# Performance work log

Hardware: AMD Instinct MI355X
Metric: run time of the kernel (lower is better)

The kernel has to match this reference:

```python
import jax, jax.numpy as jnp
import numpy as np


def _ln(x, g, b, eps=1e-5):
    m = x.mean(-1, keepdims=True)
    v = x.var(-1, keepdims=True)
    return (x - m) / jnp.sqrt(v + eps) * g + b


def setup_inputs() -> dict:
    key = jax.random.key(0)
    ks = jax.random.split(key, 12)
    B, N, F, D, DI = 1024, 100000, 128, 256, 512

    def w(k, shape, fan_in):
        return jax.random.normal(k, shape, jnp.float32) / np.sqrt(fan_in).astype(np.float32)

    return {
        "x_num": jax.random.normal(ks[0], (B, F), jnp.float32),
        "cand_num": jax.random.normal(ks[1], (N, F), jnp.float32),
        "cand_y": jax.random.normal(ks[2], (N, 1), jnp.float32),
        "W_lin": w(ks[3], (F, D), F), "b_lin": jnp.zeros(D, jnp.float32),
        "W_K": w(ks[4], (D, D), D), "b_K": jnp.zeros(D, jnp.float32),
        "W_Y": w(ks[5], (1, D), 2), "b_Y": jnp.zeros(D, jnp.float32),
        "W_T1": w(ks[6], (D, DI), D), "b_T1": jnp.zeros(DI, jnp.float32),
        "W_T2": w(ks[7], (DI, D), DI),
        "ln_p_g": jnp.ones(D, jnp.float32), "ln_p_b": jnp.zeros(D, jnp.float32),
        "W_P1": w(ks[8], (D, DI), D), "b_P1": jnp.zeros(DI, jnp.float32),
        "W_P2": w(ks[9], (DI, D), DI), "b_P2": jnp.zeros(D, jnp.float32),
        "ln_o_g": jnp.ones(D, jnp.float32), "ln_o_b": jnp.zeros(D, jnp.float32),
        "W_out": w(ks[10], (D, 1), D), "b_out": jnp.zeros(1, jnp.float32),
        "context_size": 96,
    }


def reference(x_num, cand_num, cand_y,
              W_lin, b_lin, W_K, b_K, W_Y, b_Y,
              W_T1, b_T1, W_T2,
              ln_p_g, ln_p_b, W_P1, b_P1, W_P2, b_P2,
              ln_o_g, ln_o_b, W_out, b_out,
              context_size):
    # Encoder (encoder_n_blocks=0, normlization=None -> identity f)
    x_enc = x_num @ W_lin + b_lin                       # [B, D]
    k = x_enc @ W_K + b_K                               # [B, D]
    # Candidate keys (computed under torch.no_grad in the original)
    ki_all = jax.lax.stop_gradient((cand_num @ W_lin + b_lin) @ W_K + b_K)  # [N, D]

    # Exact brute-force L2 kNN == faiss.IndexFlatL2
    d2 = (k * k).sum(-1, keepdims=True) - 2.0 * (k @ ki_all.T) + (ki_all * ki_all).sum(-1)  # [B, N]
    _, I = jax.lax.top_k(-d2, context_size)             # [B, C] ascending distance
    ki = ki_all[I]                                      # [B, C, D]

    # S = ||k - ki||^2 per the source formula; softmax over context
    S = (k * k).sum(-1, keepdims=True) \
        - 2.0 * jnp.einsum('bd,bcd->bc', k, ki) \
        + (ki * ki).sum(-1)                             # [B, C]
    weights = jax.nn.softmax(S, axis=-1)                # context_dropout=0 (eval)

    encode_y = cand_y[I] @ W_Y + b_Y                    # [B, C, D]
    diff = k[:, None, :] - ki                           # [B, C, D]
    V = encode_y + jax.nn.relu(diff @ W_T1 + b_T1) @ W_T2  # T MLP, no bias on 2nd linear
    V = jnp.einsum('bc,bcd->bd', weights, V)            # weighted context reduction

    x = x_enc + V
    # predictor residual block: LN -> Linear -> ReLU -> Linear
    h = _ln(x, ln_p_g, ln_p_b)
    x = x + (jax.nn.relu(h @ W_P1 + b_P1) @ W_P2 + b_P2)
    # head P: LN -> ReLU -> Linear(d, 1)
    return jax.nn.relu(_ln(x, ln_o_g, ln_o_b)) @ W_out + b_out  # [B, 1]
```

## Files before the change

### kernel.cpp

```cpp
#include <hip/hip_runtime.h>
#include <math.h>

#define BQ 1024
#define FDIM 128
#define DDIM 256
#define DIDIM 512
#define NTOT 100000
#define NP 100096
#define NCVT 12512
#define CTX 96
#define CAP 8192
#define MSUB 12288
#define RSUB 48
#define LBUF 1280
#define CSTR 16

typedef _Float16 f16x8 __attribute__((ext_vector_type(8)));
typedef _Float16 f16x4 __attribute__((ext_vector_type(4)));
typedef float f32x4 __attribute__((ext_vector_type(4)));

__global__ __launch_bounds__(256) void k_prep(
    const float* __restrict__ cand, _Float16* __restrict__ c2,
    const float* __restrict__ Wlin, const float* __restrict__ blin,
    const float* __restrict__ WK, const float* __restrict__ bK,
    const float* __restrict__ WT1,
    float* __restrict__ Wf, float* __restrict__ bf, float* __restrict__ WfT1)
{
    int blk = blockIdx.x, tid = threadIdx.x;
    if (blk < NCVT) {
        int t = blk*256 + tid;
        int row = t >> 5;
        int c4 = (t & 31) * 4;
        float4 v = {0.f, 0.f, 0.f, 0.f};
        if (row < NTOT) v = *(const float4*)(cand + (size_t)row*FDIM + c4);
        float vv[4] = {v.x, v.y, v.z, v.w};
        f16x4 h, hs, l;
        #pragma unroll
        for (int q = 0; q < 4; ++q) {
            _Float16 hq = (_Float16)vv[q];
            float hf = (float)hq;
            h[q]  = hq;
            hs[q] = (_Float16)(hf * 0.015625f);
            l[q]  = (_Float16)((vv[q] - hf) * 64.f);
        }
        size_t b = (size_t)row*384 + c4;
        *(f16x4*)(c2 + b)       = h;
        *(f16x4*)(c2 + b + 128) = hs;
        *(f16x4*)(c2 + b + 256) = l;
        return;
    }
    int i = blk - NCVT;
    __shared__ float red[256];
    int j = tid;
    if (i < FDIM) {
        float acc = 0.f;
        for (int l = 0; l < DDIM; ++l) acc += Wlin[i*DDIM + l] * WK[l*DDIM + j];
        Wf[i*DDIM + j] = acc;
        red[j] = acc;
        __syncthreads();
        float a0 = 0.f, a1 = 0.f;
        for (int l = 0; l < DDIM; ++l) {
            float w = red[l];
            a0 += w * WT1[(size_t)l*DIDIM + j];
            a1 += w * WT1[(size_t)l*DIDIM + j + 256];
        }
        WfT1[(size_t)i*DIDIM + j] = a0;
        WfT1[(size_t)i*DIDIM + j + 256] = a1;
    } else {
        float acc = bK[j];
        for (int l = 0; l < DDIM; ++l) acc += blin[l] * WK[l*DDIM + j];
        bf[j] = acc;
        red[j] = acc*acc; __syncthreads();
        for (int s2 = 128; s2 > 0; s2 >>= 1) { if (j < s2) red[j] += red[j+s2]; __syncthreads(); }
        if (j == 0) bf[256] = red[0];
    }
}

__global__ __launch_bounds__(256) void k_prep2(
    const float* __restrict__ x, const float* __restrict__ Wlin,
    const float* __restrict__ blin, const float* __restrict__ Wf,
    const float* __restrict__ bf, const float* __restrict__ WfT1,
    const float* __restrict__ bT1,
    float* __restrict__ xenc, float* __restrict__ kp,
    _Float16* __restrict__ kp2, float* __restrict__ xP,
    _Float16* __restrict__ Wsp)
{
    __shared__ float xs[FDIM];
    __shared__ float ks[DDIM];
    int blk = blockIdx.x, tid = threadIdx.x;
    if (blk >= BQ) {
        int jj = (blk - BQ)*2 + (tid >> 7);
        int l = tid & 127;
        float w = (jj < DDIM) ? Wf[l*DDIM + jj] : WfT1[(size_t)l*DIDIM + (jj - DDIM)];
        _Float16 h = (_Float16)w;
        float hf = (float)h;
        Wsp[(size_t)jj*384 + l]       = h;
        Wsp[(size_t)jj*384 + 128 + l] = (_Float16)((w - hf) * 64.f);
        Wsp[(size_t)jj*384 + 256 + l] = (_Float16)(hf * 0.015625f);
        return;
    }
    int b = blk, j = tid;
    if (j < FDIM) xs[j] = x[(size_t)b*FDIM + j];
    __syncthreads();
    float a0 = blin[j], a1 = bf[j];
    for (int l = 0; l < FDIM; ++l) {
        float xv = xs[l];
        a0 += xv * Wlin[l*DDIM + j];
        a1 += xv * Wf[l*DDIM + j];
    }
    xenc[(size_t)b*DDIM + j] = a0;
    ks[j] = a1;
    float p0 = bT1[j], p1 = bT1[j + 256];
    for (int l = 0; l < FDIM; ++l) {
        float xv = xs[l];
        p0 += xv * WfT1[(size_t)l*DIDIM + j];
        p1 += xv * WfT1[(size_t)l*DIDIM + j + 256];
    }
    xP[(size_t)b*DIDIM + j] = p0;
    xP[(size_t)b*DIDIM + j + 256] = p1;
    __syncthreads();
    if (j < FDIM) {
        float a = 0.f;
        for (int d = 0; d < DDIM; ++d) a += Wf[j*DDIM + d] * ks[d];
        kp[(size_t)b*FDIM + j] = a;
        _Float16 h = (_Float16)a;
        float hf = (float)h;
        kp2[(size_t)b*384 + j]       = h;
        kp2[(size_t)b*384 + 128 + j] = (_Float16)((a - hf) * 64.f);
        kp2[(size_t)b*384 + 256 + j] = (_Float16)(hf * 0.015625f);
    }
}

__global__ __launch_bounds__(256) void k_cnorm(
    const _Float16* __restrict__ A, const _Float16* __restrict__ B,
    float* __restrict__ knp, const float* __restrict__ bf)
{
    __shared__ __align__(16) _Float16 As[128*64];
    __shared__ __align__(16) _Float16 Bs[128*64];
    int tid = threadIdx.x;
    int lane = tid & 63, wv = tid >> 6;
    int wm = wv >> 1, wn = wv & 1;
    int bn = blockIdx.x * 128;
    int bm = blockIdx.y * 128;
    f32x4 acc[4][4] = {};
    const size_t baseA = (size_t)bm * 384;
    const size_t baseB = (size_t)bn * 384;
    for (int kt = 0; kt < 6; ++kt) {
        #pragma unroll
        for (int r = 0; r < 4; ++r) {
            int w = wv*4 + r;
            int s = w*64 + lane;
            int rl = s & 15;
            int q  = (s >> 4) & 3;
            int kk2= (s >> 6) & 1;
            int ii = (s >> 7) & 3;
            int wq = (s >> 9) & 1;
            size_t goff = (size_t)(wq*64 + ii*16 + rl)*384 + kt*64 + (kk2*4 + q)*8;
            __builtin_amdgcn_global_load_lds(
                (const __attribute__((address_space(1))) void*)(A + baseA + goff),
                (__attribute__((address_space(3))) void*)(As + w*512), 16, 0, 0);
            __builtin_amdgcn_global_load_lds(
                (const __attribute__((address_space(1))) void*)(B + baseB + goff),
                (__attribute__((address_space(3))) void*)(Bs + w*512), 16, 0, 0);
        }
        __syncthreads();
        #pragma unroll
        for (int kk = 0; kk < 2; ++kk) {
            f16x8 af[4], bfr[4];
            #pragma unroll
            for (int i = 0; i < 4; ++i)
                af[i] = *(const f16x8*)&As[((wm*8 + i*2 + kk)*64 + (lane>>4)*16 + (lane&15))*8];
            #pragma unroll
            for (int j = 0; j < 4; ++j)
                bfr[j] = *(const f16x8*)&Bs[((wn*8 + j*2 + kk)*64 + (lane>>4)*16 + (lane&15))*8];
            #pragma unroll
            for (int i = 0; i < 4; ++i)
                #pragma unroll
                for (int j = 0; j < 4; ++j)
                    acc[i][j] = __builtin_amdgcn_mfma_f32_16x16x32_f16(af[i], bfr[j], acc[i][j], 0, 0, 0);
        }
        __syncthreads();
    }
    float bfv[4];
    #pragma unroll
    for (int j = 0; j < 4; ++j) bfv[j] = bf[bn + wn*64 + j*16 + (lane&15)];
    int bnt = bn >> 7;
    #pragma unroll
    for (int i = 0; i < 4; ++i) {
        #pragma unroll
        for (int rg = 0; rg < 4; ++rg) {
            float s = 0.f;
            #pragma unroll
            for (int j = 0; j < 4; ++j) {
                float q = acc[i][j][rg];
                s += q * (q + 2.f*bfv[j]);
            }
            s += __shfl_xor(s, 1, 64);
            s += __shfl_xor(s, 2, 64);
            s += __shfl_xor(s, 4, 64);
            s += __shfl_xor(s, 8, 64);
            if ((lane & 15) == 0) {
                int row = bm + wm*64 + i*16 + (lane>>4)*4 + rg;
                knp[(size_t)(bnt*2 + wn)*NP + row] = s;
            }
        }
    }
}

__global__ __launch_bounds__(256) void k_norm_fin(
    const float* __restrict__ knp, const float* __restrict__ bf, float* __restrict__ kinorm)
{
    int n = blockIdx.x*256 + threadIdx.x;
    kinorm[n] = (n < NTOT)
        ? bf[256] + knp[n] + knp[(size_t)NP + n] + knp[(size_t)2*NP + n] + knp[(size_t)3*NP + n]
        : INFINITY;
}

__global__ __launch_bounds__(256) void k_mini(
    const _Float16* __restrict__ kp2, const _Float16* __restrict__ cand2,
    const float* __restrict__ kinorm, _Float16* __restrict__ msb)
{
    __shared__ __align__(16) _Float16 As[128*64];
    __shared__ __align__(16) _Float16 Bs[128*64];
    int tid = threadIdx.x;
    int lane = tid & 63, wv = tid >> 6;
    int wm = wv >> 1, wn = wv & 1;
    int bm = blockIdx.x * 128;
    int bn = blockIdx.y * 128;
    f32x4 acc[4][4] = {};
    const size_t baseA = (size_t)bm * 384;
    const size_t baseB = (size_t)bn * 384;
    for (int kt = 0; kt < 2; ++kt) {
        #pragma unroll
        for (int r = 0; r < 4; ++r) {
            int w = wv*4 + r;
            int s = w*64 + lane;
            int rl = s & 15;
            int q  = (s >> 4) & 3;
            int kk2= (s >> 6) & 1;
            int ii = (s >> 7) & 3;
            int wq = (s >> 9) & 1;
            size_t goff = (size_t)(wq*64 + ii*16 + rl)*384 + kt*64 + (kk2*4 + q)*8;
            __builtin_amdgcn_global_load_lds(
                (const __attribute__((address_space(1))) void*)(kp2 + baseA + goff),
                (__attribute__((address_space(3))) void*)(As + w*512), 16, 0, 0);
            __builtin_amdgcn_global_load_lds(
                (const __attribute__((address_space(1))) void*)(cand2 + baseB + goff),
                (__attribute__((address_space(3))) void*)(Bs + w*512), 16, 0, 0);
        }
        __syncthreads();
        #pragma unroll
        for (int kk = 0; kk < 2; ++kk) {
            f16x8 af[4], bfr[4];
            #pragma unroll
            for (int i = 0; i < 4; ++i)
                af[i] = *(const f16x8*)&As[((wm*8 + i*2 + kk)*64 + (lane>>4)*16 + (lane&15))*8];
            #pragma unroll
            for (int j = 0; j < 4; ++j)
                bfr[j] = *(const f16x8*)&Bs[((wn*8 + j*2 + kk)*64 + (lane>>4)*16 + (lane&15))*8];
            #pragma unroll
            for (int i = 0; i < 4; ++i)
                #pragma unroll
                for (int j = 0; j < 4; ++j)
                    acc[i][j] = __builtin_amdgcn_mfma_f32_16x16x32_f16(af[i], bfr[j], acc[i][j], 0, 0, 0);
        }
        __syncthreads();
    }
    #pragma unroll
    for (int i = 0; i < 4; ++i) {
        int m = bm + wm*64 + i*16 + (lane>>4)*4;
        #pragma unroll
        for (int j = 0; j < 4; ++j) {
            int nl = bn + wn*64 + j*16 + (lane&15);
            float kn = kinorm[nl];
            #pragma unroll
            for (int rg = 0; rg < 4; ++rg)
                msb[(size_t)(m + rg)*MSUB + nl] = (_Float16)fmaxf(kn - 2.f*acc[i][j][rg], 0.f);
        }
    }
}

__global__ __launch_bounds__(256) void k_subT(
    const unsigned short* __restrict__ msb, int* __restrict__ Tq, int* __restrict__ cnt)
{
    __shared__ unsigned h[1024];
    __shared__ unsigned pr[256];
    __shared__ unsigned h2[64];
    __shared__ int tstar;
    __shared__ unsigned cbel;
    int b = blockIdx.x, tid = threadIdx.x;
    if (tid == 0) cnt[b*CSTR] = 0;
    #pragma unroll
    for (int i = 0; i < 4; ++i) h[tid + i*256] = 0;
    if (tid == 0) tstar = 1023;
    if (tid < 64) h2[tid] = 0;
    __syncthreads();
    const unsigned short* row = msb + (size_t)b*MSUB;
    for (int base = 0; base < MSUB; base += 2048) {
        uint4 u = *(const uint4*)(row + base + tid*8);
        atomicAdd(&h[(u.x & 0xffffu) >> 6], 1u);
        atomicAdd(&h[(u.x >> 16) >> 6], 1u);
        atomicAdd(&h[(u.y & 0xffffu) >> 6], 1u);
        atomicAdd(&h[(u.y >> 16) >> 6], 1u);
        atomicAdd(&h[(u.z & 0xffffu) >> 6], 1u);
        atomicAdd(&h[(u.z >> 16) >> 6], 1u);
        atomicAdd(&h[(u.w & 0xffffu) >> 6], 1u);
        atomicAdd(&h[(u.w >> 16) >> 6], 1u);
    }
    __syncthreads();
    unsigned s0 = h[tid*4], s1 = h[tid*4+1], s2 = h[tid*4+2], s3 = h[tid*4+3];
    unsigned tot = s0 + s1 + s2 + s3;
    pr[tid] = tot;
    __syncthreads();
    for (int off = 1; off < 256; off <<= 1) {
        unsigned t2 = (tid >= off) ? pr[tid - off] : 0;
        __syncthreads();
        pr[tid] += t2;
        __syncthreads();
    }
    unsigned c = pr[tid] - tot;
    int found = -1;
    c += s0; if (c >= RSUB) found = tid*4;
    if (found < 0) { c += s1; if (c >= RSUB) found = tid*4+1; }
    if (found < 0) { c += s2; if (c >= RSUB) found = tid*4+2; }
    if (found < 0) { c += s3; if (c >= RSUB) found = tid*4+3; }
    if (found >= 0) atomicMin(&tstar, found);
    __syncthreads();
    if (tid == (tstar >> 2)) {
        unsigned below = pr[tid] - tot;
        int pos = tstar & 3;
        if (pos > 0) below += s0;
        if (pos > 1) below += s1;
        if (pos > 2) below += s2;
        cbel = below;
    }
    __syncthreads();
    int ts = tstar;
    for (int base = 0; base < MSUB; base += 2048) {
        uint4 u = *(const uint4*)(row + base + tid*8);
        unsigned e[8] = { u.x & 0xffffu, u.x >> 16, u.y & 0xffffu, u.y >> 16,
                          u.z & 0xffffu, u.z >> 16, u.w & 0xffffu, u.w >> 16 };
        #pragma unroll
        for (int q = 0; q < 8; ++q)
            if ((int)(e[q] >> 6) == ts) atomicAdd(&h2[e[q] & 63], 1u);
    }
    __syncthreads();
    if (tid == 0) {
        unsigned cum = cbel; int code = 63;
        for (int i = 0; i < 64; ++i) { cum += h2[i]; if (cum >= RSUB) { code = i; break; } }
        Tq[b] = (ts << 6) + code;
    }
}

__global__ __launch_bounds__(256) void k_dist_mfma(
    const _Float16* __restrict__ kp2, const _Float16* __restrict__ cand2,
    const float* __restrict__ kinorm, const int* __restrict__ Tq,
    int* __restrict__ cnt, int* __restrict__ candI)
{
    __shared__ __align__(16) _Float16 As[128*64];
    __shared__ __align__(16) _Float16 Bs[128*64];
    __shared__ int lcnt;
    __shared__ unsigned lbuf[LBUF];
    __shared__ float kns[128];
    __shared__ int tqss[128];
    int tid = threadIdx.x;
    int lane = tid & 63, wv = tid >> 6;
    int wm = wv >> 1, wn = wv & 1;
    int r0 = blockIdx.x & 7, u0 = blockIdx.x >> 3;
    int pq = r0*782 + u0;
    int bm = (pq & 7) * 128;
    int bn = (pq >> 3) * 128;
    if (tid == 0) lcnt = 0;
    if (tid < 128) { kns[tid] = kinorm[bn + tid]; tqss[tid] = Tq[bm + tid]; }
    f32x4 acc[4][4] = {};
    const size_t baseA = (size_t)bm * 384;
    const size_t baseB = (size_t)bn * 384;
    for (int kt = 0; kt < 2; ++kt) {
        #pragma unroll
        for (int r = 0; r < 4; ++r) {
            int w = wv*4 + r;
            int s = w*64 + lane;
            int rl = s & 15;
            int q  = (s >> 4) & 3;
            int kk2= (s >> 6) & 1;
            int ii = (s >> 7) & 3;
            int wq = (s >> 9) & 1;
            size_t goff = (size_t)(wq*64 + ii*16 + rl)*384 + kt*64 + (kk2*4 + q)*8;
            __builtin_amdgcn_global_load_lds(
                (const __attribute__((address_space(1))) void*)(kp2 + baseA + goff),
                (__attribute__((address_space(3))) void*)(As + w*512), 16, 0, 0);
            __builtin_amdgcn_global_load_lds(
                (const __attribute__((address_space(1))) void*)(cand2 + baseB + goff),
                (__attribute__((address_space(3))) void*)(Bs + w*512), 16, 0, 0);
        }
        __syncthreads();
        #pragma unroll
        for (int kk = 0; kk < 2; ++kk) {
            f16x8 af[4], bfr[4];
            #pragma unroll
            for (int i = 0; i < 4; ++i)
                af[i] = *(const f16x8*)&As[((wm*8 + i*2 + kk)*64 + (lane>>4)*16 + (lane&15))*8];
            #pragma unroll
            for (int j = 0; j < 4; ++j)
                bfr[j] = *(const f16x8*)&Bs[((wn*8 + j*2 + kk)*64 + (lane>>4)*16 + (lane&15))*8];
            #pragma unroll
            for (int i = 0; i < 4; ++i)
                #pragma unroll
                for (int j = 0; j < 4; ++j)
                    acc[i][j] = __builtin_amdgcn_mfma_f32_16x16x32_f16(af[i], bfr[j], acc[i][j], 0, 0, 0);
        }
        __syncthreads();
    }
    #pragma unroll
    for (int i = 0; i < 4; ++i) {
        int m0 = bm + wm*64 + i*16 + (lane>>4)*4;
        int lrow = wm*64 + i*16 + (lane>>4)*4;
        int tqs[4];
        #pragma unroll
        for (int rg = 0; rg < 4; ++rg) tqs[rg] = tqss[lrow + rg];
        #pragma unroll
        for (int j = 0; j < 4; ++j) {
            int lcol = wn*64 + j*16 + (lane&15);
            int nl = bn + lcol;
            float kn = kns[lcol];
            #pragma unroll
            for (int rg = 0; rg < 4; ++rg) {
                float sc = fmaxf(kn - 2.f*acc[i][j][rg], 0.f);
                _Float16 k16 = (_Float16)sc;
                unsigned short kb;
                __builtin_memcpy(&kb, &k16, 2);
                if (kb <= (unsigned short)tqs[rg]) {
                    int p = atomicAdd(&lcnt, 1);
                    if (p < LBUF) lbuf[p] = ((unsigned)(m0 + rg) << 17) | (unsigned)nl;
                    else {
                        int pp = atomicAdd(&cnt[(m0 + rg)*CSTR], 1);
                        if (pp < CAP) candI[(size_t)(m0 + rg)*CAP + pp] = nl;
                    }
                }
            }
        }
    }
    __syncthreads();
    int c = lcnt < LBUF ? lcnt : LBUF;
    for (int i2 = tid; i2 < c; i2 += 256) {
        unsigned pk = lbuf[i2];
        int row = pk >> 17, col = (int)(pk & 0x1ffffu);
        int pp = atomicAdd(&cnt[row*CSTR], 1);
        if (pp < CAP) candI[(size_t)row*CAP + pp] = col;
    }
}

__device__ __forceinline__ float row_score(
    const float* __restrict__ cand, const float* kps, const float* __restrict__ kinorm, int n)
{
    float acc0 = 0.f, acc1 = 0.f;
    #pragma unroll 4
    for (int d = 0; d < FDIM; d += 8) {
        float4 v0 = *(const float4*)(cand + (size_t)n*FDIM + d);
        float4 v1 = *(const float4*)(cand + (size_t)n*FDIM + d + 4);
        acc0 += v0.x*kps[d]   + v0.y*kps[d+1] + v0.z*kps[d+2] + v0.w*kps[d+3];
        acc1 += v1.x*kps[d+4] + v1.y*kps[d+5] + v1.z*kps[d+6] + v1.w*kps[d+7];
    }
    return kinorm[n] - 2.f*(acc0 + acc1);
}

__global__ __launch_bounds__(256) void k_fix(
    const float* __restrict__ kp, const float* __restrict__ cand,
    const float* __restrict__ kinorm, int* __restrict__ cnt, int* __restrict__ candI)
{
    __shared__ float kps[FDIM];
    __shared__ unsigned h[1024];
    __shared__ unsigned pr[256];
    __shared__ unsigned h2[64];
    __shared__ int tstar;
    __shared__ unsigned cbel;
    __shared__ unsigned Tsh;
    int b = blockIdx.x, tid = threadIdx.x;
    int c0 = cnt[b*CSTR];
    if (c0 >= CTX && c0 <= CAP) return;
    if (tid < FDIM) kps[tid] = kp[(size_t)b*FDIM + tid];
    #pragma unroll
    for (int i = 0; i < 4; ++i) h[tid + i*256] = 0;
    if (tid == 0) tstar = 1023;
    if (tid < 64) h2[tid] = 0;
    __syncthreads();
    for (int n = tid; n < NTOT; n += 256) {
        float sc = fmaxf(row_score(cand, kps, kinorm, n), 0.f);
        _Float16 k16 = (_Float16)sc;
        unsigned short kb; __builtin_memcpy(&kb, &k16, 2);
        atomicAdd(&h[kb >> 6], 1u);
    }
    __syncthreads();
    unsigned s0 = h[tid*4], s1 = h[tid*4+1], s2 = h[tid*4+2], s3 = h[tid*4+3];
    unsigned tot = s0 + s1 + s2 + s3;
    pr[tid] = tot;
    __syncthreads();
    for (int off = 1; off < 256; off <<= 1) {
        unsigned t2 = (tid >= off) ? pr[tid - off] : 0;
        __syncthreads();
        pr[tid] += t2;
        __syncthreads();
    }
    unsigned c = pr[tid] - tot;
    int found = -1;
    c += s0; if (c >= CTX) found = tid*4;
    if (found < 0) { c += s1; if (c >= CTX) found = tid*4+1; }
    if (found < 0) { c += s2; if (c >= CTX) found = tid*4+2; }
    if (found < 0) { c += s3; if (c >= CTX) found = tid*4+3; }
    if (found >= 0) atomicMin(&tstar, found);
    __syncthreads();
    if (tid == (tstar >> 2)) {
        unsigned below = pr[tid] - tot;
        int pos = tstar & 3;
        if (pos > 0) below += s0;
        if (pos > 1) below += s1;
        if (pos > 2) below += s2;
        cbel = below;
    }
    __syncthreads();
    int ts = tstar;
    for (int n = tid; n < NTOT; n += 256) {
        float sc = fmaxf(row_score(cand, kps, kinorm, n), 0.f);
        _Float16 k16 = (_Float16)sc;
        unsigned short kb; __builtin_memcpy(&kb, &k16, 2);
        if ((int)((unsigned)kb >> 6) == ts) atomicAdd(&h2[kb & 63], 1u);
    }
    __syncthreads();
    if (tid == 0) {
        unsigned cum = cbel; int code = 63;
        for (int i = 0; i < 64; ++i) { cum += h2[i]; if (cum >= CTX) { code = i; break; } }
        Tsh = (unsigned)((ts << 6) + code);
        cnt[b*CSTR] = 0;
    }
    __syncthreads();
    unsigned T2 = Tsh;
    for (int n = tid; n < NTOT; n += 256) {
        float sc = fmaxf(row_score(cand, kps, kinorm, n), 0.f);
        _Float16 k16 = (_Float16)sc;
        unsigned short kb; __builtin_memcpy(&kb, &k16, 2);
        if ((unsigned)kb <= T2) {
            int pp = atomicAdd(&cnt[b*CSTR], 1);
            if (pp < CAP) candI[(size_t)b*CAP + pp] = n;
        }
    }
}

__global__ __launch_bounds__(256) void k_resc(
    const float* __restrict__ kp, const float* __restrict__ cand,
    const float* __restrict__ kinorm, const int* __restrict__ cnt,
    const int* __restrict__ candI, const float* __restrict__ candy,
    int* __restrict__ finI, float* __restrict__ wts, float* __restrict__ wy)
{
    __shared__ float kps[FDIM];
    __shared__ float sval[2048];
    __shared__ int   sidx[2048];
    __shared__ float sh[256];
    int b = blockIdx.x, tid = threadIdx.x;
    if (tid < FDIM) kps[tid] = kp[(size_t)b*FDIM + tid];
    if (tid < 128) { sval[tid] = INFINITY; sidx[tid] = 0x7fffffff; }
    int nc = cnt[b*CSTR]; if (nc > CAP) nc = CAP;
    __syncthreads();
    for (int c0 = 0; c0 < nc; c0 += 1920) {
        int m = nc - c0; if (m > 1920) m = 1920;
        for (int c = tid; c < m; c += 256) {
            int n = candI[(size_t)b*CAP + c0 + c];
            sval[128 + c] = row_score(cand, kps, kinorm, n);
            sidx[128 + c] = n;
        }
        __syncthreads();
        int nv = 128 + m;
        int size = 256; while (size < nv) size <<= 1;
        for (int i2 = nv + tid; i2 < size; i2 += 256) { sval[i2] = INFINITY; sidx[i2] = 0x7fffffff; }
        __syncthreads();
        for (int k2 = 2; k2 <= size; k2 <<= 1) {
            for (int jj = k2 >> 1; jj > 0; jj >>= 1) {
                for (int i = tid; i < size; i += 256) {
                    int ix = i ^ jj;
                    if (ix > i) {
                        bool up = ((i & k2) == 0);
                        float a = sval[i], b2 = sval[ix];
                        int ia = sidx[i], ib = sidx[ix];
                        bool gt = (a > b2) || (a == b2 && ia > ib);
                        if (gt == up) {
                            sval[i] = b2; sval[ix] = a;
                            sidx[i] = ib; sidx[ix] = ia;
                        }
                    }
                }
                __syncthreads();
            }
        }
    }
    if (tid < CTX) finI[(size_t)b*CTX + tid] = sidx[tid];
    float m = sval[CTX-1];
    float e = (tid < CTX) ? expf(sval[tid] - m) : 0.f;
    sh[tid] = e;
    __syncthreads();
    for (int s2 = 128; s2 > 0; s2 >>= 1) { if (tid < s2) sh[tid] += sh[tid+s2]; __syncthreads(); }
    float sum = sh[0];
    __syncthreads();
    float w = e / sum;
    if (tid < CTX) wts[(size_t)b*CTX + tid] = w;
    sh[tid] = (tid < CTX) ? w * candy[sidx[tid]] : 0.f;
    __syncthreads();
    for (int s2 = 128; s2 > 0; s2 >>= 1) { if (tid < s2) sh[tid] += sh[tid+s2]; __syncthreads(); }
    if (tid == 0) wy[b] = sh[0];
}

__global__ __launch_bounds__(256) void k_tmlp2(
    const _Float16* __restrict__ c2, const _Float16* __restrict__ Wsp,
    const float* __restrict__ xP,
    const int* __restrict__ finI, const float* __restrict__ wts,
    float* __restrict__ Hw)
{
    __shared__ __align__(16) _Float16 As[768*8];
    __shared__ __align__(16) _Float16 Bs[1024*8];
    __shared__ int   idx[CTX];
    __shared__ float wsh[CTX];
    int b = blockIdx.x, ct = blockIdx.y;
    int tid = threadIdx.x;
    int lane = tid & 63, wv = tid >> 6;
    if (tid < CTX) { idx[tid] = finI[b*CTX + tid]; wsh[tid] = wts[b*CTX + tid]; }
    __syncthreads();
    f32x4 acc[6][2] = {};
    const _Float16* Wbase = Wsp + (size_t)(DDIM + ct*128) * 384;
    for (int kt = 0; kt < 2; ++kt) {
        #pragma unroll
        for (int w = 0; w < 3; ++w) {
            int s = (wv*3 + w)*64 + lane;
            int rl = s & 15, q = (s >> 4) & 3, kk2 = (s >> 6) & 1, ii = s >> 7;
            int grow = idx[ii*16 + rl];
            __builtin_amdgcn_global_load_lds(
                (const __attribute__((address_space(1))) void*)(c2 + (size_t)grow*384 + kt*64 + (kk2*4 + q)*8),
                (__attribute__((address_space(3))) void*)(As + (size_t)s*8), 16, 0, 0);
        }
        #pragma unroll
        for (int w = 0; w < 4; ++w) {
            int s = (wv*4 + w)*64 + lane;
            int rl = s & 15, q = (s >> 4) & 3, kk2 = (s >> 6) & 1, jj = s >> 7;
            __builtin_amdgcn_global_load_lds(
                (const __attribute__((address_space(1))) void*)(Wbase + (size_t)(jj*16 + rl)*384 + kt*64 + (kk2*4 + q)*8),
                (__attribute__((address_space(3))) void*)(Bs + (size_t)s*8), 16, 0, 0);
        }
        __syncthreads();
        #pragma unroll
        for (int kk = 0; kk < 2; ++kk) {
            f16x8 bfr[2];
            #pragma unroll
            for (int j = 0; j < 2; ++j)
                bfr[j] = *(const f16x8*)&Bs[(((wv*2 + j)*2 + kk)*64 + (lane>>4)*16 + (lane&15))*8];
            #pragma unroll
            for (int i = 0; i < 6; ++i) {
                f16x8 af = *(const f16x8*)&As[((i*2 + kk)*64 + (lane>>4)*16 + (lane&15))*8];
                #pragma unroll
                for (int j = 0; j < 2; ++j)
                    acc[i][j] = __builtin_amdgcn_mfma_f32_16x16x32_f16(af, bfr[j], acc[i][j], 0, 0, 0);
            }
        }
        __syncthreads();
    }
    #pragma unroll
    for (int j = 0; j < 2; ++j) {
        int col = ct*128 + wv*32 + j*16 + (lane & 15);
        float xv = xP[(size_t)b*DIDIM + col];
        float p = 0.f;
        #pragma unroll
        for (int i = 0; i < 6; ++i) {
            #pragma unroll
            for (int rg = 0; rg < 4; ++rg) {
                int row = i*16 + (lane>>4)*4 + rg;
                p += wsh[row] * fmaxf(xv - acc[i][j][rg], 0.f);
            }
        }
        p += __shfl_xor(p, 16, 64);
        p += __shfl_xor(p, 32, 64);
        if ((lane >> 4) == 0) Hw[(size_t)b*DIDIM + col] = p;
    }
}

__device__ __forceinline__ float bsum(float v, float* red, int j)
{
    red[j] = v; __syncthreads();
    if (j < 64) {
        float t = red[j] + red[j+64] + red[j+128] + red[j+192];
        #pragma unroll
        for (int o2 = 32; o2; o2 >>= 1) t += __shfl_xor(t, o2, 64);
        if (j == 0) red[0] = t;
    }
    __syncthreads();
    float t = red[0];
    __syncthreads();
    return t;
}

__global__ __launch_bounds__(256) void k_final4(
    const float* __restrict__ xenc, const float* __restrict__ Hw,
    const float* __restrict__ wy,
    const float* __restrict__ WY, const float* __restrict__ bY,
    const float* __restrict__ WT2,
    const float* __restrict__ lpg, const float* __restrict__ lpb,
    const float* __restrict__ WP1, const float* __restrict__ bP1,
    const float* __restrict__ WP2, const float* __restrict__ bP2,
    const float* __restrict__ logg, const float* __restrict__ lob,
    const float* __restrict__ Wout, const float* __restrict__ bout,
    float* __restrict__ out)
{
    __shared__ float hs[4][DIDIM];
    __shared__ float xs[4][DDIM];
    __shared__ float red[256];
    int b0 = blockIdx.x*4, j = threadIdx.x;
    #pragma unroll
    for (int r = 0; r < 4; ++r) {
        hs[r][j] = Hw[(size_t)(b0+r)*DIDIM + j];
        hs[r][j+256] = Hw[(size_t)(b0+r)*DIDIM + j + 256];
    }
    __syncthreads();
    float v[4];
    #pragma unroll
    for (int r = 0; r < 4; ++r) v[r] = wy[b0+r]*WY[j] + bY[j];
    for (int dd = 0; dd < DIDIM; ++dd) {
        float w = WT2[dd*DDIM + j];
        #pragma unroll
        for (int r = 0; r < 4; ++r) v[r] += hs[r][dd]*w;
    }
    float x[4];
    #pragma unroll
    for (int r = 0; r < 4; ++r) x[r] = xenc[(size_t)(b0+r)*DDIM + j] + v[r];
    #pragma unroll
    for (int r = 0; r < 4; ++r) {
        float mean = bsum(x[r], red, j) * (1.f/DDIM);
        float xc = x[r] - mean;
        float var = bsum(xc*xc, red, j) * (1.f/DDIM);
        float rstd = 1.f / sqrtf(var + 1e-5f);
        xs[r][j] = xc * rstd * lpg[j] + lpb[j];
    }
    __syncthreads();
    float u0[4], u1[4];
    #pragma unroll
    for (int r = 0; r < 4; ++r) { u0[r] = bP1[j]; u1[r] = bP1[j+256]; }
    for (int dd = 0; dd < DDIM; ++dd) {
        float w0 = WP1[(size_t)dd*DIDIM + j], w1 = WP1[(size_t)dd*DIDIM + j + 256];
        #pragma unroll
        for (int r = 0; r < 4; ++r) { float hd = xs[r][dd]; u0[r] += hd*w0; u1[r] += hd*w1; }
    }
    __syncthreads();
    #pragma unroll
    for (int r = 0; r < 4; ++r) { hs[r][j] = fmaxf(u0[r], 0.f); hs[r][j+256] = fmaxf(u1[r], 0.f); }
    __syncthreads();
    float x2[4];
    #pragma unroll
    for (int r = 0; r < 4; ++r) x2[r] = x[r] + bP2[j];
    for (int dd = 0; dd < DIDIM; ++dd) {
        float w = WP2[dd*DDIM + j];
        #pragma unroll
        for (int r = 0; r < 4; ++r) x2[r] += hs[r][dd]*w;
    }
    #pragma unroll
    for (int r = 0; r < 4; ++r) {
        float mean = bsum(x2[r], red, j) * (1.f/DDIM);
        float xc = x2[r] - mean;
        float var = bsum(xc*xc, red, j) * (1.f/DDIM);
        float rstd = 1.f / sqrtf(var + 1e-5f);
        float rr = fmaxf(xc * rstd * logg[j] + lob[j], 0.f);
        float s = bsum(rr * Wout[j], red, j);
        if (j == 0) out[b0+r] = s + bout[0];
    }
}

extern "C" void kernel_launch(void* const* d_in, const int* in_sizes, int n_in,
                              void* d_out, int out_size, void* d_ws, size_t ws_size,
                              hipStream_t stream)
{
    (void)in_sizes; (void)n_in; (void)out_size; (void)ws_size;
    const float* x_num = (const float*)d_in[0];
    const float* cand  = (const float*)d_in[1];
    const float* candy = (const float*)d_in[2];
    const float* Wlin  = (const float*)d_in[3];
    const float* blin  = (const float*)d_in[4];
    const float* WK    = (const float*)d_in[5];
    const float* bK    = (const float*)d_in[6];
    const float* WY    = (const float*)d_in[7];
    const float* bY    = (const float*)d_in[8];
    const float* WT1   = (const float*)d_in[9];
    const float* bT1   = (const float*)d_in[10];
    const float* WT2   = (const float*)d_in[11];
    const float* lpg   = (const float*)d_in[12];
    const float* lpb   = (const float*)d_in[13];
    const float* WP1   = (const float*)d_in[14];
    const float* bP1   = (const float*)d_in[15];
    const float* WP2   = (const float*)d_in[16];
    const float* bP2   = (const float*)d_in[17];
    const float* logg  = (const float*)d_in[18];
    const float* lob   = (const float*)d_in[19];
    const float* Wout  = (const float*)d_in[20];
    const float* bout  = (const float*)d_in[21];
    float* out = (float*)d_out;

    float* ws = (float*)d_ws;
    size_t o = 0;
    float* Wf     = ws + o; o += (size_t)FDIM*DDIM;
    float* bf     = ws + o; o += 320;
    float* WfT1   = ws + o; o += (size_t)FDIM*DIDIM;
    float* xenc   = ws + o; o += (size_t)BQ*DDIM;
    float* kp     = ws + o; o += (size_t)BQ*FDIM;
    float* kinorm = ws + o; o += NP;
    float* knp    = ws + o; o += (size_t)4*NP;
    int*   finI   = (int*)(ws + o); o += (size_t)BQ*CTX;
    float* wts    = ws + o; o += (size_t)BQ*CTX;
    float* wy     = ws + o; o += BQ;
    int*   Tq     = (int*)(ws + o); o += BQ;
    float* Hw     = ws + o; o += (size_t)BQ*DIDIM;
    float* xP     = ws + o; o += (size_t)BQ*DIDIM;
    _Float16* kp2 = (_Float16*)(ws + o); o += (size_t)BQ*384/2;
    _Float16* c2  = (_Float16*)(ws + o); o += (size_t)NP*384/2;
    _Float16* Wsp = (_Float16*)(ws + o); o += (size_t)768*384/2;
    int*   cnt    = (int*)(ws + o); o += (size_t)BQ*CSTR;
    int*   candI  = (int*)(ws + o); o += (size_t)BQ*CAP;
    _Float16* msb = (_Float16*)(ws + o); o += (size_t)BQ*MSUB;

    k_prep<<<dim3(NCVT + FDIM + 1), dim3(256), 0, stream>>>(
        cand, c2, Wlin, blin, WK, bK, WT1, Wf, bf, WfT1);
    k_prep2<<<dim3(BQ + 384), dim3(256), 0, stream>>>(
        x_num, Wlin, blin, Wf, bf, WfT1, bT1, xenc, kp, kp2, xP, Wsp);

    k_cnorm<<<dim3(DDIM/128, NP/128), dim3(256), 0, stream>>>(c2, Wsp, knp, bf);
    k_norm_fin<<<dim3(NP/256), dim3(256), 0, stream>>>(knp, bf, kinorm);

    k_mini<<<dim3(BQ/128, MSUB/128), dim3(256), 0, stream>>>(kp2, c2, kinorm, msb);
    k_subT<<<dim3(BQ), dim3(256), 0, stream>>>((const unsigned short*)msb, Tq, cnt);

    k_dist_mfma<<<dim3((BQ/128)*(NP/128)), dim3(256), 0, stream>>>(kp2, c2, kinorm, Tq, cnt, candI);
    k_fix<<<dim3(BQ), dim3(256), 0, stream>>>(kp, cand, kinorm, cnt, candI);
    k_resc<<<dim3(BQ), dim3(256), 0, stream>>>(kp, cand, kinorm, cnt, candI, candy,
                                               finI, wts, wy);

    k_tmlp2<<<dim3(BQ, 4), dim3(256), 0, stream>>>(c2, Wsp, xP, finI, wts, Hw);
    k_final4<<<dim3(BQ/4), dim3(256), 0, stream>>>(xenc, Hw, wy, WY, bY, WT2,
                                                   lpg, lpb, WP1, bP1, WP2, bP2,
                                                   logg, lob, Wout, bout, out);
}
```

Measured before the change: 404.0 us.

## Replace scalar final MLP kernel with split-fp16 MFMA GEMMs and LN kernels

The fused scalar FP32 kernel that ran the T2 projection, predictor MLP and output head is split into three MFMA GEMM kernels plus two per-row LayerNorm kernels. Activations and the weights WT2, WP1 and WP2 are packed into a three-part fp16 split (high, scaled high, scaled residual) so that fp16 MFMA can approximate fp32 accuracy, with weight packing added to the prep kernel. The aim is to remove the scalar FMA bottleneck in the tail. In exchange it adds extra launches, intermediate global buffers, and tiny grids (16 to 32 blocks) that may underfill the GPU.

```diff
diff --git a/kernel.cpp b/kernel.cpp
--- a/kernel.cpp
+++ b/kernel.cpp
@@ -8,6 +8,7 @@
 #define NTOT 100000
 #define NP 100096
 #define NCVT 12512
+#define NPACK 1024
 #define CTX 96
 #define CAP 8192
 #define MSUB 12288
@@ -15,6 +16,10 @@
 #define LBUF 1280
 #define CSTR 16
 
+#define WT2OFF 0
+#define WP1OFF (256*1536)
+#define WP2OFF (WP1OFF + 512*768)
+
 typedef _Float16 f16x8 __attribute__((ext_vector_type(8)));
 typedef _Float16 f16x4 __attribute__((ext_vector_type(4)));
 typedef float f32x4 __attribute__((ext_vector_type(4)));
@@ -24,7 +29,10 @@
     const float* __restrict__ Wlin, const float* __restrict__ blin,
     const float* __restrict__ WK, const float* __restrict__ bK,
     const float* __restrict__ WT1,
-    float* __restrict__ Wf, float* __restrict__ bf, float* __restrict__ WfT1)
+    const float* __restrict__ WT2, const float* __restrict__ WP1,
+    const float* __restrict__ WP2,
+    float* __restrict__ Wf, float* __restrict__ bf, float* __restrict__ WfT1,
+    _Float16* __restrict__ Wfin)
 {
     int blk = blockIdx.x, tid = threadIdx.x;
     if (blk < NCVT) {
@@ -50,6 +58,22 @@
         return;
     }
     int i = blk - NCVT;
+    if (i > FDIM) {
+        int c = i - FDIM - 1;
+        const float* W; int K, N, cl; size_t base;
+        if (c < 256)      { W = WT2; K = 512; N = 256; cl = c;     base = (size_t)WT2OFF + (size_t)c*1536; }
+        else if (c < 768) { W = WP1; K = 256; N = 512; cl = c-256; base = (size_t)WP1OFF + (size_t)(c-256)*768; }
+        else              { W = WP2; K = 512; N = 256; cl = c-768; base = (size_t)WP2OFF + (size_t)(c-768)*1536; }
+        for (int k = tid; k < K; k += 256) {
+            float w = W[(size_t)k*N + cl];
+            _Float16 h = (_Float16)w;
+            float hf = (float)h;
+            Wfin[base + k]       = h;
+            Wfin[base + K + k]   = (_Float16)((w - hf) * 64.f);
+            Wfin[base + 2*K + k] = (_Float16)(hf * 0.015625f);
+        }
+        return;
+    }
     __shared__ float red[256];
     int j = tid;
     if (i < FDIM) {
@@ -611,7 +635,7 @@
     const _Float16* __restrict__ c2, const _Float16* __restrict__ Wsp,
     const float* __restrict__ xP,
     const int* __restrict__ finI, const float* __restrict__ wts,
-    float* __restrict__ Hw)
+    _Float16* __restrict__ Hw2)
 {
     __shared__ __align__(16) _Float16 As[768*8];
     __shared__ __align__(16) _Float16 Bs[1024*8];
@@ -674,7 +698,13 @@
         }
         p += __shfl_xor(p, 16, 64);
         p += __shfl_xor(p, 32, 64);
-        if ((lane >> 4) == 0) Hw[(size_t)b*DIDIM + col] = p;
+        if ((lane >> 4) == 0) {
+            _Float16 h = (_Float16)p;
+            float hf = (float)h;
+            Hw2[(size_t)b*1536 + col]        = h;
+            Hw2[(size_t)b*1536 + 512 + col]  = (_Float16)(hf * 0.015625f);
+            Hw2[(size_t)b*1536 + 1024 + col] = (_Float16)((p - hf) * 64.f);
+        }
     }
 }
 
@@ -693,78 +723,234 @@
     return t;
 }
 
-__global__ __launch_bounds__(256) void k_final4(
-    const float* __restrict__ xenc, const float* __restrict__ Hw,
-    const float* __restrict__ wy,
+__global__ __launch_bounds__(256) void k_g1(
+    const _Float16* __restrict__ Hw2, const _Float16* __restrict__ Wfin,
+    const float* __restrict__ xenc, const float* __restrict__ wy,
     const float* __restrict__ WY, const float* __restrict__ bY,
-    const float* __restrict__ WT2,
-    const float* __restrict__ lpg, const float* __restrict__ lpb,
-    const float* __restrict__ WP1, const float* __restrict__ bP1,
-    const float* __restrict__ WP2, const float* __restrict__ bP2,
-    const float* __restrict__ logg, const float* __restrict__ lob,
-    const float* __restrict__ Wout, const float* __restrict__ bout,
-    float* __restrict__ out)
-{
-    __shared__ float hs[4][DIDIM];
-    __shared__ float xs[4][DDIM];
+    float* __restrict__ xbuf)
+{
+    __shared__ __align__(16) _Float16 As[128*64];
+    __shared__ __align__(16) _Float16 Bs[128*64];
+    int tid = threadIdx.x;
+    int lane = tid & 63, wv = tid >> 6;
+    int wm = wv >> 1, wn = wv & 1;
+    int bn = blockIdx.x * 128;
+    int bm = blockIdx.y * 128;
+    f32x4 acc[4][4] = {};
+    const size_t baseA = (size_t)bm * 1536;
+    const size_t baseB = (size_t)WT2OFF + (size_t)bn * 1536;
+    for (int kt = 0; kt < 24; ++kt) {
+        #pragma unroll
+        for (int r = 0; r < 4; ++r) {
+            int w = wv*4 + r;
+            int s = w*64 + lane;
+            int rl = s & 15, q = (s>>4)&3, kk2 = (s>>6)&1, ii = (s>>7)&3, wq = (s>>9)&1;
+            size_t goff = (size_t)(wq*64 + ii*16 + rl)*1536 + kt*64 + (kk2*4 + q)*8;
+            __builtin_amdgcn_global_load_lds(
+                (const __attribute__((address_space(1))) void*)(Hw2 + baseA + goff),
+                (__attribute__((address_space(3))) void*)(As + w*512), 16, 0, 0);
+            __builtin_amdgcn_global_load_lds(
+                (const __attribute__((address_space(1))) void*)(Wfin + baseB + goff),
+                (__attribute__((address_space(3))) void*)(Bs + w*512), 16, 0, 0);
+        }
+        __syncthreads();
+        #pragma unroll
+        for (int kk = 0; kk < 2; ++kk) {
+            f16x8 af[4], bfr[4];
+            #pragma unroll
+            for (int i = 0; i < 4; ++i)
+                af[i] = *(const f16x8*)&As[((wm*8 + i*2 + kk)*64 + (lane>>4)*16 + (lane&15))*8];
+            #pragma unroll
+            for (int j = 0; j < 4; ++j)
+                bfr[j] = *(const f16x8*)&Bs[((wn*8 + j*2 + kk)*64 + (lane>>4)*16 + (lane&15))*8];
+            #pragma unroll
+            for (int i = 0; i < 4; ++i)
+                #pragma unroll
+                for (int j = 0; j < 4; ++j)
+                    acc[i][j] = __builtin_amdgcn_mfma_f32_16x16x32_f16(af[i], bfr[j], acc[i][j], 0, 0, 0);
+        }
+        __syncthreads();
+    }
+    #pragma unroll
+    for (int i = 0; i < 4; ++i) {
+        int m = bm + wm*64 + i*16 + (lane>>4)*4;
+        #pragma unroll
+        for (int j = 0; j < 4; ++j) {
+            int n = bn + wn*64 + j*16 + (lane&15);
+            #pragma unroll
+            for (int rg = 0; rg < 4; ++rg) {
+                int row = m + rg;
+                float val = acc[i][j][rg] + xenc[(size_t)row*DDIM + n] + wy[row]*WY[n] + bY[n];
+                xbuf[(size_t)row*DDIM + n] = val;
+            }
+        }
+    }
+}
+
+__global__ __launch_bounds__(256) void k_ln1(
+    const float* __restrict__ xbuf, const float* __restrict__ lpg,
+    const float* __restrict__ lpb, _Float16* __restrict__ xs2)
+{
     __shared__ float red[256];
-    int b0 = blockIdx.x*4, j = threadIdx.x;
+    int b = blockIdx.x, j = threadIdx.x;
+    float x = xbuf[(size_t)b*DDIM + j];
+    float mean = bsum(x, red, j) * (1.f/DDIM);
+    float xc = x - mean;
+    float var = bsum(xc*xc, red, j) * (1.f/DDIM);
+    float rstd = 1.f / sqrtf(var + 1e-5f);
+    float v = xc * rstd * lpg[j] + lpb[j];
+    _Float16 h = (_Float16)v;
+    float hf = (float)h;
+    xs2[(size_t)b*768 + j]       = h;
+    xs2[(size_t)b*768 + 256 + j] = (_Float16)(hf * 0.015625f);
+    xs2[(size_t)b*768 + 512 + j] = (_Float16)((v - hf) * 64.f);
+}
+
+__global__ __launch_bounds__(256) void k_g2(
+    const _Float16* __restrict__ xs2, const _Float16* __restrict__ Wfin,
+    const float* __restrict__ bP1, _Float16* __restrict__ U2)
+{
+    __shared__ __align__(16) _Float16 As[128*64];
+    __shared__ __align__(16) _Float16 Bs[128*64];
+    int tid = threadIdx.x;
+    int lane = tid & 63, wv = tid >> 6;
+    int wm = wv >> 1, wn = wv & 1;
+    int bn = blockIdx.x * 128;
+    int bm = blockIdx.y * 128;
+    f32x4 acc[4][4] = {};
+    const size_t baseA = (size_t)bm * 768;
+    const size_t baseB = (size_t)WP1OFF + (size_t)bn * 768;
+    for (int kt = 0; kt < 12; ++kt) {
+        #pragma unroll
+        for (int r = 0; r < 4; ++r) {
+            int w = wv*4 + r;
+            int s = w*64 + lane;
+            int rl = s & 15, q = (s>>4)&3, kk2 = (s>>6)&1, ii = (s>>7)&3, wq = (s>>9)&1;
+            size_t goff = (size_t)(wq*64 + ii*16 + rl)*768 + kt*64 + (kk2*4 + q)*8;
+            __builtin_amdgcn_global_load_lds(
+                (const __attribute__((address_space(1))) void*)(xs2 + baseA + goff),
+                (__attribute__((address_space(3))) void*)(As + w*512), 16, 0, 0);
+            __builtin_amdgcn_global_load_lds(
+                (const __attribute__((address_space(1))) void*)(Wfin + baseB + goff),
+                (__attribute__((address_space(3))) void*)(Bs + w*512), 16, 0, 0);
+        }
+        __syncthreads();
+        #pragma unroll
+        for (int kk = 0; kk < 2; ++kk) {
+            f16x8 af[4], bfr[4];
+            #pragma unroll
+            for (int i = 0; i < 4; ++i)
+                af[i] = *(const f16x8*)&As[((wm*8 + i*2 + kk)*64 + (lane>>4)*16 + (lane&15))*8];
+            #pragma unroll
+            for (int j = 0; j < 4; ++j)
+                bfr[j] = *(const f16x8*)&Bs[((wn*8 + j*2 + kk)*64 + (lane>>4)*16 + (lane&15))*8];
+            #pragma unroll
+            for (int i = 0; i < 4; ++i)
+                #pragma unroll
+                for (int j = 0; j < 4; ++j)
+                    acc[i][j] = __builtin_amdgcn_mfma_f32_16x16x32_f16(af[i], bfr[j], acc[i][j], 0, 0, 0);
+        }
+        __syncthreads();
+    }
     #pragma unroll
-    for (int r = 0; r < 4; ++r) {
-        hs[r][j] = Hw[(size_t)(b0+r)*DIDIM + j];
-        hs[r][j+256] = Hw[(size_t)(b0+r)*DIDIM + j + 256];
-    }
-    __syncthreads();
-    float v[4];
+    for (int i = 0; i < 4; ++i) {
+        int m = bm + wm*64 + i*16 + (lane>>4)*4;
+        #pragma unroll
+        for (int j = 0; j < 4; ++j) {
+            int n = bn + wn*64 + j*16 + (lane&15);
+            float bv = bP1[n];
+            #pragma unroll
+            for (int rg = 0; rg < 4; ++rg) {
+                int row = m + rg;
+                float r = fmaxf(acc[i][j][rg] + bv, 0.f);
+                _Float16 h = (_Float16)r;
+                float hf = (float)h;
+                U2[(size_t)row*1536 + n]        = h;
+                U2[(size_t)row*1536 + 512 + n]  = (_Float16)(hf * 0.015625f);
+                U2[(size_t)row*1536 + 1024 + n] = (_Float16)((r - hf) * 64.f);
+            }
+        }
+    }
+}
+
+__global__ __launch_bounds__(256) void k_g3(
+    const _Float16* __restrict__ U2, const _Float16* __restrict__ Wfin,
+    const float* __restrict__ xbuf, const float* __restrict__ bP2,
+    float* __restrict__ x2buf)
+{
+    __shared__ __align__(16) _Float16 As[128*64];
+    __shared__ __align__(16) _Float16 Bs[128*64];
+    int tid = threadIdx.x;
+    int lane = tid & 63, wv = tid >> 6;
+    int wm = wv >> 1, wn = wv & 1;
+    int bn = blockIdx.x * 128;
+    int bm = blockIdx.y * 128;
+    f32x4 acc[4][4] = {};
+    const size_t baseA = (size_t)bm * 1536;
+    const size_t baseB = (size_t)WP2OFF + (size_t)bn * 1536;
+    for (int kt = 0; kt < 24; ++kt) {
+        #pragma unroll
+        for (int r = 0; r < 4; ++r) {
+            int w = wv*4 + r;
+            int s = w*64 + lane;
+            int rl = s & 15, q = (s>>4)&3, kk2 = (s>>6)&1, ii = (s>>7)&3, wq = (s>>9)&1;
+            size_t goff = (size_t)(wq*64 + ii*16 + rl)*1536 + kt*64 + (kk2*4 + q)*8;
+            __builtin_amdgcn_global_load_lds(
+                (const __attribute__((address_space(1))) void*)(U2 + baseA + goff),
+                (__attribute__((address_space(3))) void*)(As + w*512), 16, 0, 0);
+            __builtin_amdgcn_global_load_lds(
+                (const __attribute__((address_space(1))) void*)(Wfin + baseB + goff),
+                (__attribute__((address_space(3))) void*)(Bs + w*512), 16, 0, 0);
+        }
+        __syncthreads();
+        #pragma unroll
+        for (int kk = 0; kk < 2; ++kk) {
+            f16x8 af[4], bfr[4];
+            #pragma unroll
+            for (int i = 0; i < 4; ++i)
+                af[i] = *(const f16x8*)&As[((wm*8 + i*2 + kk)*64 + (lane>>4)*16 + (lane&15))*8];
+            #pragma unroll
+            for (int j = 0; j < 4; ++j)
+                bfr[j] = *(const f16x8*)&Bs[((wn*8 + j*2 + kk)*64 + (lane>>4)*16 + (lane&15))*8];
+            #pragma unroll
+            for (int i = 0; i < 4; ++i)
+                #pragma unroll
+                for (int j = 0; j < 4; ++j)
+                    acc[i][j] = __builtin_amdgcn_mfma_f32_16x16x32_f16(af[i], bfr[j], acc[i][j], 0, 0, 0);
+        }
+        __syncthreads();
+    }
     #pragma unroll
-    for (int r = 0; r < 4; ++r) v[r] = wy[b0+r]*WY[j] + bY[j];
-    for (int dd = 0; dd < DIDIM; ++dd) {
-        float w = WT2[dd*DDIM + j];
-        #pragma unroll
-        for (int r = 0; r < 4; ++r) v[r] += hs[r][dd]*w;
-    }
-    float x[4];
-    #pragma unroll
-    for (int r = 0; r < 4; ++r) x[r] = xenc[(size_t)(b0+r)*DDIM + j] + v[r];
-    #pragma unroll
-    for (int r = 0; r < 4; ++r) {
-        float mean = bsum(x[r], red, j) * (1.f/DDIM);
-        float xc = x[r] - mean;
-        float var = bsum(xc*xc, red, j) * (1.f/DDIM);
-        float rstd = 1.f / sqrtf(var + 1e-5f);
-        xs[r][j] = xc * rstd * lpg[j] + lpb[j];
-    }
-    __syncthreads();
-    float u0[4], u1[4];
-    #pragma unroll
-    for (int r = 0; r < 4; ++r) { u0[r] = bP1[j]; u1[r] = bP1[j+256]; }
-    for (int dd = 0; dd < DDIM; ++dd) {
-        float w0 = WP1[(size_t)dd*DIDIM + j], w1 = WP1[(size_t)dd*DIDIM + j + 256];
-        #pragma unroll
-        for (int r = 0; r < 4; ++r) { float hd = xs[r][dd]; u0[r] += hd*w0; u1[r] += hd*w1; }
-    }
-    __syncthreads();
-    #pragma unroll
-    for (int r = 0; r < 4; ++r) { hs[r][j] = fmaxf(u0[r], 0.f); hs[r][j+256] = fmaxf(u1[r], 0.f); }
-    __syncthreads();
-    float x2[4];
-    #pragma unroll
-    for (int r = 0; r < 4; ++r) x2[r] = x[r] + bP2[j];
-    for (int dd = 0; dd < DIDIM; ++dd) {
-        float w = WP2[dd*DDIM + j];
-        #pragma unroll
-        for (int r = 0; r < 4; ++r) x2[r] += hs[r][dd]*w;
-    }
-    #pragma unroll
-    for (int r = 0; r < 4; ++r) {
-        float mean = bsum(x2[r], red, j) * (1.f/DDIM);
-        float xc = x2[r] - mean;
-        float var = bsum(xc*xc, red, j) * (1.f/DDIM);
-        float rstd = 1.f / sqrtf(var + 1e-5f);
-        float rr = fmaxf(xc * rstd * logg[j] + lob[j], 0.f);
-        float s = bsum(rr * Wout[j], red, j);
-        if (j == 0) out[b0+r] = s + bout[0];
-    }
+    for (int i = 0; i < 4; ++i) {
+        int m = bm + wm*64 + i*16 + (lane>>4)*4;
+        #pragma unroll
+        for (int j = 0; j < 4; ++j) {
+            int n = bn + wn*64 + j*16 + (lane&15);
+            float bv = bP2[n];
+            #pragma unroll
+            for (int rg = 0; rg < 4; ++rg) {
+                int row = m + rg;
+                x2buf[(size_t)row*DDIM + n] = acc[i][j][rg] + xbuf[(size_t)row*DDIM + n] + bv;
+            }
+        }
+    }
+}
+
+__global__ __launch_bounds__(256) void k_out(
+    const float* __restrict__ x2buf, const float* __restrict__ logg,
+    const float* __restrict__ lob, const float* __restrict__ Wout,
+    const float* __restrict__ bout, float* __restrict__ out)
+{
+    __shared__ float red[256];
+    int b = blockIdx.x, j = threadIdx.x;
+    float x = x2buf[(size_t)b*DDIM + j];
+    float mean = bsum(x, red, j) * (1.f/DDIM);
+    float xc = x - mean;
+    float var = bsum(xc*xc, red, j) * (1.f/DDIM);
+    float rstd = 1.f / sqrtf(var + 1e-5f);
+    float rr = fmaxf(xc * rstd * logg[j] + lob[j], 0.f);
+    float s = bsum(rr * Wout[j], red, j);
+    if (j == 0) out[b] = s + bout[0];
 }
 
 extern "C" void kernel_launch(void* const* d_in, const int* in_sizes, int n_in,
@@ -809,17 +995,22 @@
     float* wts    = ws + o; o += (size_t)BQ*CTX;
     float* wy     = ws + o; o += BQ;
     int*   Tq     = (int*)(ws + o); o += BQ;
-    float* Hw     = ws + o; o += (size_t)BQ*DIDIM;
     float* xP     = ws + o; o += (size_t)BQ*DIDIM;
+    float* xbuf   = ws + o; o += (size_t)BQ*DDIM;
+    float* x2buf  = ws + o; o += (size_t)BQ*DDIM;
     _Float16* kp2 = (_Float16*)(ws + o); o += (size_t)BQ*384/2;
     _Float16* c2  = (_Float16*)(ws + o); o += (size_t)NP*384/2;
     _Float16* Wsp = (_Float16*)(ws + o); o += (size_t)768*384/2;
+    _Float16* Wfin= (_Float16*)(ws + o); o += (size_t)(WP2OFF + 256*1536)/2;
+    _Float16* Hw2 = (_Float16*)(ws + o); o += (size_t)BQ*1536/2;
+    _Float16* xs2 = (_Float16*)(ws + o); o += (size_t)BQ*768/2;
+    _Float16* U2  = (_Float16*)(ws + o); o += (size_t)BQ*1536/2;
     int*   cnt    = (int*)(ws + o); o += (size_t)BQ*CSTR;
     int*   candI  = (int*)(ws + o); o += (size_t)BQ*CAP;
     _Float16* msb = (_Float16*)(ws + o); o += (size_t)BQ*MSUB;
 
-    k_prep<<<dim3(NCVT + FDIM + 1), dim3(256), 0, stream>>>(
-        cand, c2, Wlin, blin, WK, bK, WT1, Wf, bf, WfT1);
+    k_prep<<<dim3(NCVT + FDIM + 1 + NPACK), dim3(256), 0, stream>>>(
+        cand, c2, Wlin, blin, WK, bK, WT1, WT2, WP1, WP2, Wf, bf, WfT1, Wfin);
     k_prep2<<<dim3(BQ + 384), dim3(256), 0, stream>>>(
         x_num, Wlin, blin, Wf, bf, WfT1, bT1, xenc, kp, kp2, xP, Wsp);
 
@@ -834,8 +1025,11 @@
     k_resc<<<dim3(BQ), dim3(256), 0, stream>>>(kp, cand, kinorm, cnt, candI, candy,
                                                finI, wts, wy);
 
-    k_tmlp2<<<dim3(BQ, 4), dim3(256), 0, stream>>>(c2, Wsp, xP, finI, wts, Hw);
-    k_final4<<<dim3(BQ/4), dim3(256), 0, stream>>>(xenc, Hw, wy, WY, bY, WT2,
-                                                   lpg, lpb, WP1, bP1, WP2, bP2,
-                                                   logg, lob, Wout, bout, out);
-}
+    k_tmlp2<<<dim3(BQ, 4), dim3(256), 0, stream>>>(c2, Wsp, xP, finI, wts, Hw2);
+
+    k_g1<<<dim3(2, 8), dim3(256), 0, stream>>>(Hw2, Wfin, xenc, wy, WY, bY, xbuf);
+    k_ln1<<<dim3(BQ), dim3(256), 0, stream>>>(xbuf, lpg, lpb, xs2);
+    k_g2<<<dim3(4, 8), dim3(256), 0, stream>>>(xs2, Wfin, bP1, U2);
+    k_g3<<<dim3(2, 8), dim3(256), 0, stream>>>(U2, Wfin, xbuf, bP2, x2buf);
+    k_out<<<dim3(BQ), dim3(256), 0, stream>>>(x2buf, logg, lob, Wout, bout, out);
+}
```

After: 457.9 us. 1.13x slower.
